# Kernel tuning notes

Hardware: AMD Instinct MI355X
Metric: run time of the kernel (lower is better)

Reference implementation:

```python
import jax, jax.numpy as jnp
import numpy as np
from jax import lax

B = 32768
L = 200          # window_size
K = 5            # conv kernel
CIN = 6
FLAT = L - K + 1  # 196, conv1d valid output length (out channels = 1)


def setup_inputs() -> dict:
    key = jax.random.key(0)
    ks = jax.random.split(key, 9)
    s = lambda *sh: 1.0 / np.sqrt(sh[-1])
    x = jax.random.normal(ks[0], (B, CIN, L), dtype=jnp.float32)
    conv_w = jax.random.normal(ks[1], (1, CIN, K), dtype=jnp.float32) * (1.0 / np.sqrt(CIN * K))
    conv_b = jax.random.normal(ks[2], (1,), dtype=jnp.float32) * 0.1
    w1 = jax.random.normal(ks[3], (FLAT, 50), dtype=jnp.float32) * (1.0 / np.sqrt(FLAT))
    b1 = jax.random.normal(ks[4], (50,), dtype=jnp.float32) * 0.1
    w2 = jax.random.normal(ks[5], (50, 30), dtype=jnp.float32) * (1.0 / np.sqrt(50))
    b2 = jax.random.normal(ks[6], (30,), dtype=jnp.float32) * 0.1
    w3 = jax.random.normal(ks[7], (30, 15), dtype=jnp.float32) * (1.0 / np.sqrt(30))
    b3 = jax.random.normal(ks[8], (15,), dtype=jnp.float32) * 0.1
    return {"x": x, "conv_w": conv_w, "conv_b": conv_b, "w1": w1, "b1": b1,
            "w2": w2, "b2": b2, "w3": w3, "b3": b3}


def reference(x, conv_w, conv_b, w1, b1, w2, b2, w3, b3):
    # conv1d (valid): [B,6,200] -> [B,1,196]
    y = lax.conv_general_dilated(x, conv_w, window_strides=(1,), padding='VALID',
                                 dimension_numbers=('NCH', 'OIH', 'NCH'))
    y = y + conv_b[None, :, None]
    h = y.reshape(x.shape[0], -1)                       # [B,196]
    h = jax.nn.relu(h @ w1 + b1)                        # [B,50]
    h = jax.nn.relu(h @ w2 + b2)                        # [B,30]
    out = h @ w3 + b3                                   # [B,15]
    # Procrustes orthogonalization of the 3x3 block
    R = out[:, :9].reshape(-1, 3, 3)
    U, _, VT = jnp.linalg.svd(R)                        # batched 3x3 SVD
    det = jnp.linalg.det(jnp.matmul(U, VT))             # [B]
    scale = jnp.stack([jnp.ones_like(det), jnp.ones_like(det), det], axis=1)  # diag(1,1,det)
    R_norm = jnp.matmul(U, VT * scale[:, :, None])      # U @ S @ VT
    return jnp.concatenate([R_norm.reshape(-1, 9), out[:, 9:]], axis=1)
```

## Files before the change

kernel.cpp:

```cpp
#include <hip/hip_runtime.h>
#include <math.h>

#define BATCH 32768
#define LW    200
#define CIN   6
#define KSZ   5
#define FLAT  196
#define NH1   50
#define NH2   30
#define NOUT  15

__global__ __launch_bounds__(256) void conv_kernel(
    const float* __restrict__ x, const float* __restrict__ cw,
    const float* __restrict__ cb, float* __restrict__ co)
{
    int t = blockIdx.x * 256 + threadIdx.x;
    int b = t / 49;
    int q = t - b * 49;
    int i0 = q * 4;

    float w[CIN][KSZ];
#pragma unroll
    for (int c = 0; c < CIN; ++c)
#pragma unroll
        for (int k = 0; k < KSZ; ++k) w[c][k] = cw[c * KSZ + k];
    float bias = cb[0];

    float acc0 = bias, acc1 = bias, acc2 = bias, acc3 = bias;
    const float* xb = x + (long)b * (CIN * LW) + i0;
#pragma unroll
    for (int c = 0; c < CIN; ++c) {
        float4 lo = *(const float4*)(xb + c * LW);
        float4 hi = *(const float4*)(xb + c * LW + 4);
        float xf[8] = {lo.x, lo.y, lo.z, lo.w, hi.x, hi.y, hi.z, hi.w};
#pragma unroll
        for (int k = 0; k < KSZ; ++k) {
            acc0 = fmaf(xf[k + 0], w[c][k], acc0);
            acc1 = fmaf(xf[k + 1], w[c][k], acc1);
            acc2 = fmaf(xf[k + 2], w[c][k], acc2);
            acc3 = fmaf(xf[k + 3], w[c][k], acc3);
        }
    }
    *(float4*)(co + (long)b * FLAT + i0) = make_float4(acc0, acc1, acc2, acc3);
}

__global__ __launch_bounds__(256) void mlp_kernel(
    const float* __restrict__ co,
    const float* __restrict__ w1, const float* __restrict__ b1,
    const float* __restrict__ w2, const float* __restrict__ b2,
    const float* __restrict__ w3, const float* __restrict__ b3,
    float* __restrict__ out)
{
    __shared__ float part[3][64][52];

    int tid  = threadIdx.x;
    int wv   = __builtin_amdgcn_readfirstlane(tid >> 6);
    int lane = tid & 63;
    int b    = blockIdx.x * 64 + lane;
    int ibase = wv * 49;

    float cl[49];
    const float* crow = co + (long)b * FLAT + ibase;
#pragma unroll
    for (int ii = 0; ii < 49; ++ii) cl[ii] = crow[ii];

    float h1p[NH1];
#pragma unroll
    for (int j = 0; j < NH1; ++j) h1p[j] = 0.f;

#pragma unroll
    for (int ii = 0; ii < 49; ++ii) {
        float c = cl[ii];
        const float* row = w1 + (ibase + ii) * NH1;
#pragma unroll
        for (int j = 0; j < NH1; ++j) h1p[j] = fmaf(c, row[j], h1p[j]);
    }

    if (wv != 0) {
#pragma unroll
        for (int j = 0; j < NH1; ++j) part[wv - 1][lane][j] = h1p[j];
    }
    __syncthreads();
    if (wv != 0) return;

    float h1[NH1];
#pragma unroll
    for (int j = 0; j < NH1; ++j) {
        float s = h1p[j] + part[0][lane][j] + part[1][lane][j] + part[2][lane][j] + b1[j];
        h1[j] = fmaxf(s, 0.f);
    }

    float h2[NH2];
#pragma unroll
    for (int j = 0; j < NH2; ++j) h2[j] = b2[j];
#pragma unroll
    for (int k = 0; k < NH1; ++k) {
        float hk = h1[k];
        const float* row = w2 + k * NH2;
#pragma unroll
        for (int j = 0; j < NH2; ++j) h2[j] = fmaf(hk, row[j], h2[j]);
    }
#pragma unroll
    for (int j = 0; j < NH2; ++j) h2[j] = fmaxf(h2[j], 0.f);

    float o[NOUT];
#pragma unroll
    for (int j = 0; j < NOUT; ++j) o[j] = b3[j];
#pragma unroll
    for (int k = 0; k < NH2; ++k) {
        float hk = h2[k];
        const float* row = w3 + k * NOUT;
#pragma unroll
        for (int j = 0; j < NOUT; ++j) o[j] = fmaf(hk, row[j], o[j]);
    }

    {
        double r00 = (double)o[0], r01 = (double)o[1], r02 = (double)o[2];
        double r10 = (double)o[3], r11 = (double)o[4], r12 = (double)o[5];
        double r20 = (double)o[6], r21 = (double)o[7], r22 = (double)o[8];

        double A[4][4], V[4][4];
        A[0][0] = r00 + r11 + r22;
        A[1][1] = r00 - r11 - r22;
        A[2][2] = r11 - r00 - r22;
        A[3][3] = r22 - r00 - r11;
        A[0][1] = A[1][0] = r21 - r12;
        A[0][2] = A[2][0] = r02 - r20;
        A[0][3] = A[3][0] = r10 - r01;
        A[1][2] = A[2][1] = r01 + r10;
        A[1][3] = A[3][1] = r02 + r20;
        A[2][3] = A[3][2] = r12 + r21;
#pragma unroll
        for (int i = 0; i < 4; ++i)
#pragma unroll
            for (int j = 0; j < 4; ++j) V[i][j] = (i == j) ? 1.0 : 0.0;

        const int pr[6][2] = {{0,1},{0,2},{0,3},{1,2},{1,3},{2,3}};
        for (int sweep = 0; sweep < 6; ++sweep) {
#pragma unroll
            for (int pi = 0; pi < 6; ++pi) {
                const int p = pr[pi][0], q = pr[pi][1];
                double apq = A[p][q];
                if (apq != 0.0) {
                    double theta = (A[q][q] - A[p][p]) / (2.0 * apq);
                    double t = copysign(1.0, theta) / (fabs(theta) + sqrt(1.0 + theta * theta));
                    double c = 1.0 / sqrt(1.0 + t * t);
                    double s = t * c;
#pragma unroll
                    for (int k = 0; k < 4; ++k) {
                        double akp = A[k][p], akq = A[k][q];
                        A[k][p] = c * akp - s * akq;
                        A[k][q] = s * akp + c * akq;
                    }
#pragma unroll
                    for (int k = 0; k < 4; ++k) {
                        double apk = A[p][k], aqk = A[q][k];
                        A[p][k] = c * apk - s * aqk;
                        A[q][k] = s * apk + c * aqk;
                    }
#pragma unroll
                    for (int k = 0; k < 4; ++k) {
                        double vkp = V[k][p], vkq = V[k][q];
                        V[k][p] = c * vkp - s * vkq;
                        V[k][q] = s * vkp + c * vkq;
                    }
                }
            }
        }

        int best = 0;
        double bl = A[0][0];
#pragma unroll
        for (int i = 1; i < 4; ++i) {
            if (A[i][i] > bl) { bl = A[i][i]; best = i; }
        }
        double vw = V[0][best], vx = V[1][best], vy = V[2][best], vz = V[3][best];
        double inv = 1.0 / sqrt(vw * vw + vx * vx + vy * vy + vz * vz);
        vw *= inv; vx *= inv; vy *= inv; vz *= inv;

        double xx = vx * vx, yy = vy * vy, zz = vz * vz;
        double xy = vx * vy, xz = vx * vz, yz = vy * vz;
        double wx = vw * vx, wy = vw * vy, wz = vw * vz;

        float* ob = out + (long)b * NOUT;
        ob[0]  = (float)(1.0 - 2.0 * (yy + zz));
        ob[1]  = (float)(2.0 * (xy - wz));
        ob[2]  = (float)(2.0 * (xz + wy));
        ob[3]  = (float)(2.0 * (xy + wz));
        ob[4]  = (float)(1.0 - 2.0 * (xx + zz));
        ob[5]  = (float)(2.0 * (yz - wx));
        ob[6]  = (float)(2.0 * (xz - wy));
        ob[7]  = (float)(2.0 * (yz + wx));
        ob[8]  = (float)(1.0 - 2.0 * (xx + yy));
        ob[9]  = o[9];
        ob[10] = o[10];
        ob[11] = o[11];
        ob[12] = o[12];
        ob[13] = o[13];
        ob[14] = o[14];
    }
}

extern "C" void kernel_launch(void* const* d_in, const int* in_sizes, int n_in,
                              void* d_out, int out_size, void* d_ws, size_t ws_size,
                              hipStream_t stream) {
    const float* x  = (const float*)d_in[0];
    const float* cw = (const float*)d_in[1];
    const float* cb = (const float*)d_in[2];
    const float* w1 = (const float*)d_in[3];
    const float* b1 = (const float*)d_in[4];
    const float* w2 = (const float*)d_in[5];
    const float* b2 = (const float*)d_in[6];
    const float* w3 = (const float*)d_in[7];
    const float* b3 = (const float*)d_in[8];
    float* outp = (float*)d_out;
    float* co   = (float*)d_ws;

    conv_kernel<<<(BATCH * 49) / 256, 256, 0, stream>>>(x, cw, cb, co);
    mlp_kernel<<<BATCH / 64, 256, 0, stream>>>(co, w1, b1, w2, b2, w3, b3, outp);
}
```

Measured before the change: 302.7 us.

## Use fp32 Jacobi eigen-solve and single-wave MLP without split-K reduction

Measured after the change: 331.5 us. 1.1x slower.

```diff
diff --git a/kernel.cpp b/kernel.cpp
--- a/kernel.cpp
+++ b/kernel.cpp
@@ -44,51 +44,33 @@
     *(float4*)(co + (long)b * FLAT + i0) = make_float4(acc0, acc1, acc2, acc3);
 }
 
-__global__ __launch_bounds__(256) void mlp_kernel(
+__global__ __launch_bounds__(64) void mlp_kernel(
     const float* __restrict__ co,
     const float* __restrict__ w1, const float* __restrict__ b1,
     const float* __restrict__ w2, const float* __restrict__ b2,
     const float* __restrict__ w3, const float* __restrict__ b3,
     float* __restrict__ out)
 {
-    __shared__ float part[3][64][52];
-
-    int tid  = threadIdx.x;
-    int wv   = __builtin_amdgcn_readfirstlane(tid >> 6);
-    int lane = tid & 63;
-    int b    = blockIdx.x * 64 + lane;
-    int ibase = wv * 49;
-
-    float cl[49];
-    const float* crow = co + (long)b * FLAT + ibase;
-#pragma unroll
-    for (int ii = 0; ii < 49; ++ii) cl[ii] = crow[ii];
-
-    float h1p[NH1];
-#pragma unroll
-    for (int j = 0; j < NH1; ++j) h1p[j] = 0.f;
-
-#pragma unroll
-    for (int ii = 0; ii < 49; ++ii) {
-        float c = cl[ii];
-        const float* row = w1 + (ibase + ii) * NH1;
-#pragma unroll
-        for (int j = 0; j < NH1; ++j) h1p[j] = fmaf(c, row[j], h1p[j]);
-    }
-
-    if (wv != 0) {
-#pragma unroll
-        for (int j = 0; j < NH1; ++j) part[wv - 1][lane][j] = h1p[j];
-    }
-    __syncthreads();
-    if (wv != 0) return;
+    int b = blockIdx.x * 64 + threadIdx.x;
 
     float h1[NH1];
 #pragma unroll
-    for (int j = 0; j < NH1; ++j) {
-        float s = h1p[j] + part[0][lane][j] + part[1][lane][j] + part[2][lane][j] + b1[j];
-        h1[j] = fmaxf(s, 0.f);
-    }
+    for (int j = 0; j < NH1; ++j) h1[j] = b1[j];
+
+    const float4* c4p = (const float4*)(co + (size_t)b * FLAT);
+    for (int k = 0; k < FLAT / 4; ++k) {
+        float4 c4 = c4p[k];
+        float cv[4] = {c4.x, c4.y, c4.z, c4.w};
+#pragma unroll
+        for (int r = 0; r < 4; ++r) {
+            const float* row = w1 + (4 * k + r) * NH1;
+            float c = cv[r];
+#pragma unroll
+            for (int j = 0; j < NH1; ++j) h1[j] = fmaf(c, row[j], h1[j]);
+        }
+    }
+#pragma unroll
+    for (int j = 0; j < NH1; ++j) h1[j] = fmaxf(h1[j], 0.f);
 
     float h2[NH2];
 #pragma unroll
@@ -115,11 +97,11 @@
     }
 
     {
-        double r00 = (double)o[0], r01 = (double)o[1], r02 = (double)o[2];
-        double r10 = (double)o[3], r11 = (double)o[4], r12 = (double)o[5];
-        double r20 = (double)o[6], r21 = (double)o[7], r22 = (double)o[8];
-
-        double A[4][4], V[4][4];
+        float r00 = o[0], r01 = o[1], r02 = o[2];
+        float r10 = o[3], r11 = o[4], r12 = o[5];
+        float r20 = o[6], r21 = o[7], r22 = o[8];
+
+        float A[4][4], V[4][4];
         A[0][0] = r00 + r11 + r22;
         A[1][1] = r00 - r11 - r22;
         A[2][2] = r11 - r00 - r22;
@@ -133,34 +115,34 @@
 #pragma unroll
         for (int i = 0; i < 4; ++i)
 #pragma unroll
-            for (int j = 0; j < 4; ++j) V[i][j] = (i == j) ? 1.0 : 0.0;
+            for (int j = 0; j < 4; ++j) V[i][j] = (i == j) ? 1.f : 0.f;
 
         const int pr[6][2] = {{0,1},{0,2},{0,3},{1,2},{1,3},{2,3}};
-        for (int sweep = 0; sweep < 6; ++sweep) {
+        for (int sweep = 0; sweep < 7; ++sweep) {
 #pragma unroll
             for (int pi = 0; pi < 6; ++pi) {
                 const int p = pr[pi][0], q = pr[pi][1];
-                double apq = A[p][q];
-                if (apq != 0.0) {
-                    double theta = (A[q][q] - A[p][p]) / (2.0 * apq);
-                    double t = copysign(1.0, theta) / (fabs(theta) + sqrt(1.0 + theta * theta));
-                    double c = 1.0 / sqrt(1.0 + t * t);
-                    double s = t * c;
+                float apq = A[p][q];
+                if (fabsf(apq) > 1e-20f) {
+                    float theta = (A[q][q] - A[p][p]) / (2.f * apq);
+                    float t = copysignf(1.f, theta) / (fabsf(theta) + sqrtf(1.f + theta * theta));
+                    float c = rsqrtf(1.f + t * t);
+                    float s = t * c;
 #pragma unroll
                     for (int k = 0; k < 4; ++k) {
-                        double akp = A[k][p], akq = A[k][q];
+                        float akp = A[k][p], akq = A[k][q];
                         A[k][p] = c * akp - s * akq;
                         A[k][q] = s * akp + c * akq;
                     }
 #pragma unroll
                     for (int k = 0; k < 4; ++k) {
-                        double apk = A[p][k], aqk = A[q][k];
+                        float apk = A[p][k], aqk = A[q][k];
                         A[p][k] = c * apk - s * aqk;
                         A[q][k] = s * apk + c * aqk;
                     }
 #pragma unroll
                     for (int k = 0; k < 4; ++k) {
-                        double vkp = V[k][p], vkq = V[k][q];
+                        float vkp = V[k][p], vkq = V[k][q];
                         V[k][p] = c * vkp - s * vkq;
                         V[k][q] = s * vkp + c * vkq;
                     }
@@ -169,29 +151,29 @@
         }
 
         int best = 0;
-        double bl = A[0][0];
-#pragma unroll
-        for (int i = 1; i < 4; ++i) {
+        float bl = A[0][0];
+#pragma unroll
+        for (int i = 1; i < 4; ++i)
             if (A[i][i] > bl) { bl = A[i][i]; best = i; }
-        }
-        double vw = V[0][best], vx = V[1][best], vy = V[2][best], vz = V[3][best];
-        double inv = 1.0 / sqrt(vw * vw + vx * vx + vy * vy + vz * vz);
+
+        float vw = V[0][best], vx = V[1][best], vy = V[2][best], vz = V[3][best];
+        float inv = rsqrtf(vw * vw + vx * vx + vy * vy + vz * vz);
         vw *= inv; vx *= inv; vy *= inv; vz *= inv;
 
-        double xx = vx * vx, yy = vy * vy, zz = vz * vz;
-        double xy = vx * vy, xz = vx * vz, yz = vy * vz;
-        double wx = vw * vx, wy = vw * vy, wz = vw * vz;
+        float xx = vx * vx, yy = vy * vy, zz = vz * vz;
+        float xy = vx * vy, xz = vx * vz, yz = vy * vz;
+        float wx = vw * vx, wy = vw * vy, wz = vw * vz;
 
         float* ob = out + (long)b * NOUT;
-        ob[0]  = (float)(1.0 - 2.0 * (yy + zz));
-        ob[1]  = (float)(2.0 * (xy - wz));
-        ob[2]  = (float)(2.0 * (xz + wy));
-        ob[3]  = (float)(2.0 * (xy + wz));
-        ob[4]  = (float)(1.0 - 2.0 * (xx + zz));
-        ob[5]  = (float)(2.0 * (yz - wx));
-        ob[6]  = (float)(2.0 * (xz - wy));
-        ob[7]  = (float)(2.0 * (yz + wx));
-        ob[8]  = (float)(1.0 - 2.0 * (xx + yy));
+        ob[0]  = 1.f - 2.f * (yy + zz);
+        ob[1]  = 2.f * (xy - wz);
+        ob[2]  = 2.f * (xz + wy);
+        ob[3]  = 2.f * (xy + wz);
+        ob[4]  = 1.f - 2.f * (xx + zz);
+        ob[5]  = 2.f * (yz - wx);
+        ob[6]  = 2.f * (xz - wy);
+        ob[7]  = 2.f * (yz + wx);
+        ob[8]  = 1.f - 2.f * (xx + yy);
         ob[9]  = o[9];
         ob[10] = o[10];
         ob[11] = o[11];
@@ -217,5 +199,5 @@
     float* co   = (float*)d_ws;
 
     conv_kernel<<<(BATCH * 49) / 256, 256, 0, stream>>>(x, cw, cb, co);
-    mlp_kernel<<<BATCH / 64, 256, 0, stream>>>(co, w1, b1, w2, b2, w3, b3, outp);
+    mlp_kernel<<<BATCH / 64, 64, 0, stream>>>(co, w1, b1, w2, b2, w3, b3, outp);
 }
```
